# Optimization experiments

Hardware: AMD Instinct MI355X
Metric: run time of the kernel (lower is better)

## Reference

```python
import jax, jax.numpy as jnp
import numpy as np

TEMPERATURES = (0.02, 0.05, 0.2)
NORMALIZE_FEATURES = True
NORMALIZE_DRIFT = True
EPS = 1e-8


def _sqdist(a, b):
    # ||a_i - b_j||^2 via expansion; clamp tiny negatives from fp error
    aa = jnp.sum(a * a, axis=1)[:, None]
    bb = jnp.sum(b * b, axis=1)[None, :]
    return jnp.maximum(aa + bb - 2.0 * (a @ b.T), 0.0)


def compute_drifting_field(x, y_pos, y_neg, temperatures):
    """Multi-scale RBF-kernel drifting field.

    V(x) = mean_tau [ softmax_j(-d(x,y_pos_j)/tau) @ y_pos
                    - softmax_k(-d(x,y_neg_k)/tau) @ y_neg ]
    (the attraction/repulsion (y - x) terms: the -x cancels between pos and neg)
    Returns (V, raw_drift_norm, lambda_V).
    """
    D = x.shape[1]
    if NORMALIZE_FEATURES:
        # scale-invariant distances: global RMS of the reference samples
        ref = jnp.concatenate([y_pos, y_neg], axis=0)
        scale = jnp.sqrt(jnp.mean(ref * ref) + EPS)
    else:
        scale = jnp.asarray(1.0, x.dtype)
    xs, yp, yn = x / scale, y_pos / scale, y_neg / scale

    d_pos = _sqdist(xs, yp)  # [N, N_pos]
    d_neg = _sqdist(xs, yn)  # [N, N_neg]

    V = jnp.zeros_like(xs)
    for tau in temperatures:
        w_pos = jax.nn.softmax(-d_pos / tau, axis=1)
        w_neg = jax.nn.softmax(-d_neg / tau, axis=1)
        V = V + (w_pos @ yp - w_neg @ yn)
    V = (V / len(temperatures)) * scale  # back to original feature scale

    raw_drift_norm = jnp.mean(jnp.sum(V * V, axis=1))  # E[||V_raw||^2]
    lambda_V = jnp.sqrt(raw_drift_norm / D + EPS)
    if NORMALIZE_DRIFT:
        V = V / lambda_V
    return V, raw_drift_norm, lambda_V


def reference(x, y_pos, y_neg):
    V, raw_drift_norm, lambda_V = compute_drifting_field(x, y_pos, y_neg, TEMPERATURES)
    x_target = jax.lax.stop_gradient(x + V)
    loss_per_sample = jnp.mean((x - x_target) ** 2, axis=1)
    loss = jnp.mean(loss_per_sample)  # reduction='mean'
    drift_norm = jnp.mean(jnp.sum(V * V, axis=1))
    # per-temperature logging: original redundantly recomputes the full field
    per_temp = jnp.stack([
        compute_drifting_field(x, y_pos, y_neg, (tau,))[1] for tau in TEMPERATURES
    ])
    return loss, drift_norm, raw_drift_norm, lambda_V, per_temp, jax.lax.stop_gradient(V)


def setup_inputs() -> dict:
    key = jax.random.key(0)
    k1, k2, k3 = jax.random.split(key, 3)
    N, D = 4096, 256
    return {
        "x": jax.random.normal(k1, (N, D), dtype=jnp.float32),
        "y_pos": jax.random.normal(k2, (N, D), dtype=jnp.float32),
        "y_neg": jax.random.normal(k3, (N, D), dtype=jnp.float32),
    }
```

## Files before the change

### kernel.cpp

```cpp
#include <hip/hip_runtime.h>

#define NPTS 4096
#define DIM  256
#define TIL  64
#define WCAND 32

typedef unsigned short u16;
typedef unsigned long long u64;
typedef __attribute__((ext_vector_type(8))) short bf16x8;
typedef __attribute__((ext_vector_type(4))) float f32x4;
typedef __attribute__((ext_vector_type(4))) unsigned short u16x4;

__device__ __forceinline__ float exp2fast(float x) {
  float r;
  asm("v_exp_f32 %0, %1" : "=v"(r) : "v"(x));
  return r;
}

__device__ __forceinline__ void gload_lds16(const void* g, void* l) {
  __builtin_amdgcn_global_load_lds((const __attribute__((address_space(1))) void*)g,
                                   (__attribute__((address_space(3))) void*)l, 16, 0, 0);
}

__device__ __forceinline__ float blk_sum(float v, float* sh) {
  #pragma unroll
  for (int off = 32; off; off >>= 1) v += __shfl_down(v, off);
  int lane = threadIdx.x & 63, w = threadIdx.x >> 6;
  __syncthreads();
  if (lane == 0) sh[w] = v;
  __syncthreads();
  return sh[0] + sh[1] + sh[2] + sh[3];
}

__global__ __launch_bounds__(256) void split3_kernel(
    const float* __restrict__ x, const float* __restrict__ yp, const float* __restrict__ yn,
    u16* __restrict__ xb, u16* __restrict__ ypb, u16* __restrict__ ynb,
    float* __restrict__ bbp, float* __restrict__ bbn)
{
  const float* src; u16* dst; float* bb;
  if      (blockIdx.y == 0) { src = x;  dst = xb;  bb = nullptr; }
  else if (blockIdx.y == 1) { src = yp; dst = ypb; bb = bbp; }
  else                      { src = yn; dst = ynb; bb = bbn; }

  int lane = threadIdx.x & 63;
  int wave = threadIdx.x >> 6;
  int row  = blockIdx.x * 4 + wave;
  const float4 v = *reinterpret_cast<const float4*>(src + (size_t)row * DIM + lane * 4);
  float xs[4] = {v.x, v.y, v.z, v.w};
  u16x4 h;
  float ss = 0.f;
  #pragma unroll
  for (int e = 0; e < 4; ++e) {
    unsigned b = __float_as_uint(xs[e]);
    h[e] = (u16)((b + 0x7fffu + ((b >> 16) & 1u)) >> 16);
    ss += xs[e] * xs[e];
  }
  *reinterpret_cast<u16x4*>(dst + (size_t)row * DIM + lane * 4) = h;
  if (bb) {
    #pragma unroll
    for (int off = 32; off; off >>= 1) ss += __shfl_down(ss, off);
    if (lane == 0) bb[row] = ss;
  }
}

__global__ __launch_bounds__(256) void reduce_ss(
    const float* __restrict__ bbp, const float* __restrict__ bbn, float* __restrict__ accums)
{
  __shared__ float red[4];
  int tid = threadIdx.x;
  float s = 0.f;
  for (int k = tid; k < NPTS; k += 256) s += bbp[k] + bbn[k];
  s = blk_sum(s, red);
  if (tid == 0) accums[0] = s;
}

__global__ __launch_bounds__(256, 4) void gemm_kernel(
    const u16* __restrict__ Xb, const u16* __restrict__ Ypb, const u16* __restrict__ Ynb,
    const float* __restrict__ bbp, const float* __restrict__ bbn,
    const float* __restrict__ accums,
    float* __restrict__ M, u64* __restrict__ Kmask)
{
  __shared__ u16 Ah[2][128 * 32];
  __shared__ u16 Bh[2][128 * 32];

  const int side = blockIdx.z;
  const u16* Yb = side ? Ynb : Ypb;
  const float* bbv = side ? bbn : bbp;

  const int tid  = threadIdx.x;
  const int lane = tid & 63;
  const int wave = tid >> 6;
  const int wm = wave >> 1, wn = wave & 1;
  const int l15 = lane & 15, lhi = lane >> 4;

  const int rf = blockIdx.x * 128;
  const int cf = blockIdx.y * 128;
  const int til = blockIdx.y * 2 + wn;

  const int r0  = tid >> 2;
  const int pc0 = tid & 3;
  const int r1  = (tid + 256) >> 2;
  const int pc1 = tid & 3;

  f32x4 acc[4][4] = {};

  {
    int gc0 = pc0 ^ (r0 & 3), gc1 = pc1 ^ (r1 & 3);
    gload_lds16(Xb + (size_t)(rf + r0) * DIM + gc0 * 8, Ah[0] + r0 * 32 + pc0 * 8);
    gload_lds16(Yb + (size_t)(cf + r0) * DIM + gc0 * 8, Bh[0] + r0 * 32 + pc0 * 8);
    gload_lds16(Xb + (size_t)(rf + r1) * DIM + gc1 * 8, Ah[0] + r1 * 32 + pc1 * 8);
    gload_lds16(Yb + (size_t)(cf + r1) * DIM + gc1 * 8, Bh[0] + r1 * 32 + pc1 * 8);
  }

  #pragma unroll 2
  for (int ks = 0; ks < 8; ++ks) {
    const int cur = ks & 1;
    if (ks < 7) asm volatile("s_waitcnt vmcnt(4)" ::: "memory");
    else        asm volatile("s_waitcnt vmcnt(0)" ::: "memory");
    __builtin_amdgcn_s_barrier();

    if (ks < 7) {
      int ko = (ks + 1) * 32;
      int gc0 = pc0 ^ (r0 & 3), gc1 = pc1 ^ (r1 & 3);
      gload_lds16(Xb + (size_t)(rf + r0) * DIM + ko + gc0 * 8, Ah[cur ^ 1] + r0 * 32 + pc0 * 8);
      gload_lds16(Yb + (size_t)(cf + r0) * DIM + ko + gc0 * 8, Bh[cur ^ 1] + r0 * 32 + pc0 * 8);
      gload_lds16(Xb + (size_t)(rf + r1) * DIM + ko + gc1 * 8, Ah[cur ^ 1] + r1 * 32 + pc1 * 8);
      gload_lds16(Yb + (size_t)(cf + r1) * DIM + ko + gc1 * 8, Bh[cur ^ 1] + r1 * 32 + pc1 * 8);
    }

    bf16x8 a[4], b[4];
    #pragma unroll
    for (int mi = 0; mi < 4; ++mi) {
      int R = wm * 64 + mi * 16 + l15;
      a[mi] = *reinterpret_cast<const bf16x8*>(Ah[cur] + R * 32 + ((lhi ^ (R & 3)) * 8));
    }
    #pragma unroll
    for (int ni = 0; ni < 4; ++ni) {
      int R = wn * 64 + ni * 16 + l15;
      b[ni] = *reinterpret_cast<const bf16x8*>(Bh[cur] + R * 32 + ((lhi ^ (R & 3)) * 8));
    }
    #pragma unroll
    for (int mi = 0; mi < 4; ++mi)
      #pragma unroll
      for (int ni = 0; ni < 4; ++ni)
        acc[mi][ni] = __builtin_amdgcn_mfma_f32_16x16x32_bf16(a[mi], b[ni], acc[mi][ni], 0, 0, 0);
  }

  const float scalesq = accums[0] * (1.0f / (2.0f * NPTS * DIM)) + 1e-8f;
  const float thrP = 30.0f * scalesq * 0.2f + 2.5f * scalesq + 0.5f;

  float bbc[4];
  #pragma unroll
  for (int ni = 0; ni < 4; ++ni) bbc[ni] = bbv[cf + wn * 64 + ni * 16 + l15];

  #pragma unroll
  for (int mi = 0; mi < 4; ++mi)
    #pragma unroll
    for (int r = 0; r < 4; ++r) {
      float uv[4];
      float mx = -3.0e38f;
      #pragma unroll
      for (int ni = 0; ni < 4; ++ni) {
        uv[ni] = 2.0f * acc[mi][ni][r] - bbc[ni];
        mx = fmaxf(mx, uv[ni]);
      }
      #pragma unroll
      for (int off = 1; off < 16; off <<= 1) mx = fmaxf(mx, __shfl_xor(mx, off));
      const float cut = mx - thrP;

      u64 bal[4];
      #pragma unroll
      for (int ni = 0; ni < 4; ++ni) bal[ni] = __ballot(uv[ni] > cut);

      u64 mask = 0;
      #pragma unroll
      for (int ni = 0; ni < 4; ++ni)
        mask |= ((bal[ni] >> (lhi * 16)) & 0xFFFFull) << (ni * 16);

      const int rowG = rf + wm * 64 + mi * 16 + lhi * 4 + r;
      if (l15 == 0) {
        Kmask[((size_t)side * TIL + til) * NPTS + rowG] = mask;
        M[((size_t)side * NPTS + rowG) * TIL + til] = mx;
      }
    }
}

__global__ __launch_bounds__(256) void row_kernel(
    const float* __restrict__ M, const u64* __restrict__ Kmask,
    const float* __restrict__ bbp, const float* __restrict__ bbn,
    const float* __restrict__ x,
    const float* __restrict__ ypos, const float* __restrict__ yneg,
    const float* __restrict__ accums, float* __restrict__ parts,
    float* __restrict__ Vout)
{
  __shared__ unsigned cl[4][WCAND];

  const int tid  = threadIdx.x;
  const int lane = tid & 63;
  const int w    = tid >> 6;
  const int row  = blockIdx.x * 4 + w;

  const float scalesq = accums[0] * (1.0f / (2.0f * NPTS * DIM)) + 1e-8f;
  const float L2E = 1.4426950408889634f;
  const float c0 = L2E / (scalesq * 0.02f);
  const float c1 = L2E / (scalesq * 0.05f);
  const float c2 = L2E / (scalesq * 0.2f);
  const float thrP = 30.0f * scalesq * 0.2f + 2.5f * scalesq + 0.5f;

  const f32x4 xv = *reinterpret_cast<const f32x4*>(x + (size_t)row * DIM + lane * 4);

  f32x4 V0 = {0,0,0,0}, V1 = {0,0,0,0}, V2 = {0,0,0,0};

  for (int side = 0; side < 2; ++side) {
    const float* bb = side ? bbn : bbp;
    const float* y  = side ? yneg : ypos;
    const float sgn = side ? -1.f : 1.f;

    float Mv = M[((size_t)side * NPTS + row) * TIL + lane];
    float g = Mv;
    #pragma unroll
    for (int off = 32; off; off >>= 1) g = fmaxf(g, __shfl_xor(g, off));
    const float cut = g - thrP;

    u64 mm = __ballot(Mv > cut);
    int nc = 0;
    while (mm) {
      int t = __ffsll((long long)mm) - 1;
      mm &= mm - 1;
      u64 mask = Kmask[((size_t)side * TIL + t) * NPTS + row];
      bool keep = (mask >> lane) & 1ull;
      int rank = __popcll(mask & ((1ull << lane) - 1ull));
      if (keep && nc + rank < WCAND) cl[w][nc + rank] = t * 64 + lane;
      nc += __popcll(mask);
    }
    nc = nc < WCAND ? nc : WCAND;

    float me = -3.0e38f, p0 = 0.f, p1 = 0.f, p2 = 0.f;
    f32x4 A0 = {0,0,0,0}, A1 = {0,0,0,0}, A2 = {0,0,0,0};
    for (int bs = 0; bs < nc; bs += 8) {
      const int rem = nc - bs;
      int jq[8];
      f32x4 yv[8];
      float dq[8], uq[8];
      #pragma unroll
      for (int q = 0; q < 8; ++q) {
        int idx = (q < rem) ? bs + q : bs;
        jq[q] = (int)cl[w][idx];
        yv[q] = *reinterpret_cast<const f32x4*>(y + (size_t)jq[q] * DIM + lane * 4);
      }
      #pragma unroll
      for (int q = 0; q < 8; ++q)
        dq[q] = xv[0]*yv[q][0] + xv[1]*yv[q][1] + xv[2]*yv[q][2] + xv[3]*yv[q][3];
      #pragma unroll
      for (int off = 32; off; off >>= 1)
        #pragma unroll
        for (int q = 0; q < 8; ++q) dq[q] += __shfl_xor(dq[q], off);
      #pragma unroll
      for (int q = 0; q < 8; ++q)
        uq[q] = (q < rem) ? 2.0f * dq[q] - bb[jq[q]] : -3.0e38f;

      float cm = uq[0];
      #pragma unroll
      for (int q = 1; q < 8; ++q) cm = fmaxf(cm, uq[q]);
      float nm = fmaxf(me, cm);
      float s0 = exp2fast((me - nm) * c0);
      float s1 = exp2fast((me - nm) * c1);
      float s2 = exp2fast((me - nm) * c2);
      p0 *= s0; p1 *= s1; p2 *= s2;
      A0 *= s0; A1 *= s1; A2 *= s2;
      #pragma unroll
      for (int q = 0; q < 8; ++q) {
        float du = uq[q] - nm;
        float e0 = exp2fast(du * c0);
        float e1 = exp2fast(du * c1);
        float e2 = exp2fast(du * c2);
        p0 += e0; p1 += e1; p2 += e2;
        A0 += e0 * yv[q]; A1 += e1 * yv[q]; A2 += e2 * yv[q];
      }
      me = nm;
    }
    V0 += (sgn / p0) * A0;
    V1 += (sgn / p1) * A1;
    V2 += (sgn / p2) * A2;
  }

  f32x4 vr = (V0 + V1 + V2) * (1.0f / 3.0f);
  *reinterpret_cast<f32x4*>(Vout + (size_t)row * DIM + lane * 4) = vr;

  float s0 = V0[0]*V0[0] + V0[1]*V0[1] + V0[2]*V0[2] + V0[3]*V0[3];
  float s1 = V1[0]*V1[0] + V1[1]*V1[1] + V1[2]*V1[2] + V1[3]*V1[3];
  float s2 = V2[0]*V2[0] + V2[1]*V2[1] + V2[2]*V2[2] + V2[3]*V2[3];
  float sr = vr[0]*vr[0] + vr[1]*vr[1] + vr[2]*vr[2] + vr[3]*vr[3];
  #pragma unroll
  for (int off = 32; off; off >>= 1) {
    s0 += __shfl_xor(s0, off);
    s1 += __shfl_xor(s1, off);
    s2 += __shfl_xor(s2, off);
    sr += __shfl_xor(sr, off);
  }
  if (lane == 0) {
    parts[row]            = sr;
    parts[NPTS + row]     = s0;
    parts[2 * NPTS + row] = s1;
    parts[3 * NPTS + row] = s2;
  }
}

__global__ __launch_bounds__(256) void reduce_parts(
    const float* __restrict__ parts, float* __restrict__ accums)
{
  __shared__ float red[4];
  int tid = threadIdx.x;
  #pragma unroll
  for (int a = 0; a < 4; ++a) {
    float s = 0.f;
    for (int k = tid; k < NPTS; k += 256) s += parts[a * NPTS + k];
    s = blk_sum(s, red);
    if (tid == 0) accums[1 + a] = s;
  }
}

__global__ __launch_bounds__(256) void final_kernel(
    const float* __restrict__ accums, float* __restrict__ out)
{
  float raw  = accums[1] * (1.0f / NPTS);
  float lam2 = raw * (1.0f / DIM) + 1e-8f;
  float lam  = sqrtf(lam2);
  float inv  = 1.0f / lam;
  size_t idx = (size_t)blockIdx.x * 256 + threadIdx.x;
  out[7 + idx] *= inv;
  if (blockIdx.x == 0 && threadIdx.x == 0) {
    float drift = raw / lam2;
    out[0] = drift * (1.0f / DIM);
    out[1] = drift;
    out[2] = raw;
    out[3] = lam;
    out[4] = accums[2] * (1.0f / NPTS);
    out[5] = accums[3] * (1.0f / NPTS);
    out[6] = accums[4] * (1.0f / NPTS);
  }
}

extern "C" void kernel_launch(void* const* d_in, const int* in_sizes, int n_in,
                              void* d_out, int out_size, void* d_ws, size_t ws_size,
                              hipStream_t stream)
{
  (void)in_sizes; (void)n_in; (void)out_size; (void)ws_size;
  const float* x    = (const float*)d_in[0];
  const float* ypos = (const float*)d_in[1];
  const float* yneg = (const float*)d_in[2];
  float* out = (float*)d_out;
  char* ws = (char*)d_ws;

  float* accums = (float*)ws;
  float* bbp    = (float*)(ws + 256);
  float* bbn    = (float*)(ws + 16640);
  float* parts  = (float*)(ws + 33024);
  float* M      = (float*)(ws + 98560);
  u64*   Kmask  = (u64*)(ws + 98560 + 2097152);
  u16* xb  = (u16*)(ws + 98560 + 2097152 + 4194304);
  u16* ypb = xb + (size_t)NPTS * DIM;
  u16* ynb = xb + 2 * (size_t)NPTS * DIM;

  split3_kernel<<<dim3(NPTS / 4, 3), 256, 0, stream>>>(x, ypos, yneg, xb, ypb, ynb, bbp, bbn);
  reduce_ss<<<1, 256, 0, stream>>>(bbp, bbn, accums);
  gemm_kernel<<<dim3(32, 32, 2), 256, 0, stream>>>(xb, ypb, ynb, bbp, bbn, accums, M, Kmask);
  row_kernel<<<NPTS / 4, 256, 0, stream>>>(M, Kmask, bbp, bbn, x, ypos, yneg,
                                           accums, parts, out + 7);
  reduce_parts<<<1, 256, 0, stream>>>(parts, accums);
  final_kernel<<<NPTS, 256, 0, stream>>>(accums, out);
}
```

Before: 86.36 us.

## Fold reduction kernels into consumers, triple-buffer GEMM loads, swizzle block order

Drops the single-block reduce_ss and reduce_parts launches. Each GEMM and row block now redundantly sums the 8192 row norms to get the scale, and final_kernel recomputes the drift-norm reduction in every block. The GEMM moves from double to triple-buffered LDS with a two-stage prefetch, lowers the occupancy hint from 4 to 3, and remaps block IDs for better L2 locality. The aim is fewer serialized tiny launches and better latency hiding, at the cost of redundant reduction work in every block and more LDS per block.

```diff
diff --git a/kernel.cpp b/kernel.cpp
--- a/kernel.cpp
+++ b/kernel.cpp
@@ -30,6 +30,19 @@
   if (lane == 0) sh[w] = v;
   __syncthreads();
   return sh[0] + sh[1] + sh[2] + sh[3];
+}
+
+__device__ __forceinline__ float block_scalesq(
+    const float* __restrict__ bbp, const float* __restrict__ bbn, float* red, int tid) {
+  float s = 0.f;
+  #pragma unroll
+  for (int q = 0; q < 4; ++q) {
+    f32x4 a = *reinterpret_cast<const f32x4*>(bbp + (q * 256 + tid) * 4);
+    f32x4 b = *reinterpret_cast<const f32x4*>(bbn + (q * 256 + tid) * 4);
+    s += a[0] + a[1] + a[2] + a[3] + b[0] + b[1] + b[2] + b[3];
+  }
+  float tot = blk_sum(s, red);
+  return tot * (1.0f / (2.0f * NPTS * DIM)) + 1e-8f;
 }
 
 __global__ __launch_bounds__(256) void split3_kernel(
@@ -63,70 +76,64 @@
   }
 }
 
-__global__ __launch_bounds__(256) void reduce_ss(
-    const float* __restrict__ bbp, const float* __restrict__ bbn, float* __restrict__ accums)
-{
-  __shared__ float red[4];
-  int tid = threadIdx.x;
-  float s = 0.f;
-  for (int k = tid; k < NPTS; k += 256) s += bbp[k] + bbn[k];
-  s = blk_sum(s, red);
-  if (tid == 0) accums[0] = s;
-}
-
-__global__ __launch_bounds__(256, 4) void gemm_kernel(
+__global__ __launch_bounds__(256, 3) void gemm_kernel(
     const u16* __restrict__ Xb, const u16* __restrict__ Ypb, const u16* __restrict__ Ynb,
     const float* __restrict__ bbp, const float* __restrict__ bbn,
-    const float* __restrict__ accums,
     float* __restrict__ M, u64* __restrict__ Kmask)
 {
-  __shared__ u16 Ah[2][128 * 32];
-  __shared__ u16 Bh[2][128 * 32];
-
-  const int side = blockIdx.z;
+  __shared__ u16 Ah[3][128 * 32];
+  __shared__ u16 Bh[3][128 * 32];
+  __shared__ float red[4];
+
+  const int tid  = threadIdx.x;
+
+  const unsigned lid = blockIdx.x + (blockIdx.y << 5) + (blockIdx.z << 10);
+  const unsigned swz = (lid & 7) * 256 + (lid >> 3);
+  const int bx = swz & 31, by = (swz >> 5) & 31, side = (int)(swz >> 10);
+
   const u16* Yb = side ? Ynb : Ypb;
   const float* bbv = side ? bbn : bbp;
 
-  const int tid  = threadIdx.x;
+  const float scalesq = block_scalesq(bbp, bbn, red, tid);
+
   const int lane = tid & 63;
   const int wave = tid >> 6;
   const int wm = wave >> 1, wn = wave & 1;
   const int l15 = lane & 15, lhi = lane >> 4;
 
-  const int rf = blockIdx.x * 128;
-  const int cf = blockIdx.y * 128;
-  const int til = blockIdx.y * 2 + wn;
+  const int rf = bx * 128;
+  const int cf = by * 128;
+  const int til = by * 2 + wn;
 
   const int r0  = tid >> 2;
-  const int pc0 = tid & 3;
   const int r1  = (tid + 256) >> 2;
-  const int pc1 = tid & 3;
+  const int pc  = tid & 3;
+  const int gc0 = pc ^ (r0 & 3);
+  const int gc1 = pc ^ (r1 & 3);
 
   f32x4 acc[4][4] = {};
 
-  {
-    int gc0 = pc0 ^ (r0 & 3), gc1 = pc1 ^ (r1 & 3);
-    gload_lds16(Xb + (size_t)(rf + r0) * DIM + gc0 * 8, Ah[0] + r0 * 32 + pc0 * 8);
-    gload_lds16(Yb + (size_t)(cf + r0) * DIM + gc0 * 8, Bh[0] + r0 * 32 + pc0 * 8);
-    gload_lds16(Xb + (size_t)(rf + r1) * DIM + gc1 * 8, Ah[0] + r1 * 32 + pc1 * 8);
-    gload_lds16(Yb + (size_t)(cf + r1) * DIM + gc1 * 8, Bh[0] + r1 * 32 + pc1 * 8);
-  }
-
-  #pragma unroll 2
+#define STAGE(KS, BUF)                                                                    \
+  do {                                                                                    \
+    int ko_ = (KS) * 32;                                                                  \
+    gload_lds16(Xb + (size_t)(rf + r0) * DIM + ko_ + gc0 * 8, Ah[BUF] + r0 * 32 + pc * 8);\
+    gload_lds16(Yb + (size_t)(cf + r0) * DIM + ko_ + gc0 * 8, Bh[BUF] + r0 * 32 + pc * 8);\
+    gload_lds16(Xb + (size_t)(rf + r1) * DIM + ko_ + gc1 * 8, Ah[BUF] + r1 * 32 + pc * 8);\
+    gload_lds16(Yb + (size_t)(cf + r1) * DIM + ko_ + gc1 * 8, Bh[BUF] + r1 * 32 + pc * 8);\
+  } while (0)
+
+  STAGE(0, 0);
+  STAGE(1, 1);
+
+  #pragma unroll 1
   for (int ks = 0; ks < 8; ++ks) {
-    const int cur = ks & 1;
+    const int cur = ks % 3;
     if (ks < 7) asm volatile("s_waitcnt vmcnt(4)" ::: "memory");
     else        asm volatile("s_waitcnt vmcnt(0)" ::: "memory");
     __builtin_amdgcn_s_barrier();
-
-    if (ks < 7) {
-      int ko = (ks + 1) * 32;
-      int gc0 = pc0 ^ (r0 & 3), gc1 = pc1 ^ (r1 & 3);
-      gload_lds16(Xb + (size_t)(rf + r0) * DIM + ko + gc0 * 8, Ah[cur ^ 1] + r0 * 32 + pc0 * 8);
-      gload_lds16(Yb + (size_t)(cf + r0) * DIM + ko + gc0 * 8, Bh[cur ^ 1] + r0 * 32 + pc0 * 8);
-      gload_lds16(Xb + (size_t)(rf + r1) * DIM + ko + gc1 * 8, Ah[cur ^ 1] + r1 * 32 + pc1 * 8);
-      gload_lds16(Yb + (size_t)(cf + r1) * DIM + ko + gc1 * 8, Bh[cur ^ 1] + r1 * 32 + pc1 * 8);
-    }
+    __builtin_amdgcn_sched_barrier(0);
+
+    if (ks < 6) STAGE(ks + 2, (ks + 2) % 3);
 
     bf16x8 a[4], b[4];
     #pragma unroll
@@ -145,8 +152,8 @@
       for (int ni = 0; ni < 4; ++ni)
         acc[mi][ni] = __builtin_amdgcn_mfma_f32_16x16x32_bf16(a[mi], b[ni], acc[mi][ni], 0, 0, 0);
   }
-
-  const float scalesq = accums[0] * (1.0f / (2.0f * NPTS * DIM)) + 1e-8f;
+#undef STAGE
+
   const float thrP = 30.0f * scalesq * 0.2f + 2.5f * scalesq + 0.5f;
 
   float bbc[4];
@@ -190,17 +197,17 @@
     const float* __restrict__ bbp, const float* __restrict__ bbn,
     const float* __restrict__ x,
     const float* __restrict__ ypos, const float* __restrict__ yneg,
-    const float* __restrict__ accums, float* __restrict__ parts,
-    float* __restrict__ Vout)
+    float* __restrict__ parts, float* __restrict__ Vout)
 {
   __shared__ unsigned cl[4][WCAND];
+  __shared__ float red[4];
 
   const int tid  = threadIdx.x;
   const int lane = tid & 63;
   const int w    = tid >> 6;
   const int row  = blockIdx.x * 4 + w;
 
-  const float scalesq = accums[0] * (1.0f / (2.0f * NPTS * DIM)) + 1e-8f;
+  const float scalesq = block_scalesq(bbp, bbn, red, tid);
   const float L2E = 1.4426950408889634f;
   const float c0 = L2E / (scalesq * 0.02f);
   const float c1 = L2E / (scalesq * 0.05f);
@@ -306,38 +313,37 @@
   }
 }
 
-__global__ __launch_bounds__(256) void reduce_parts(
-    const float* __restrict__ parts, float* __restrict__ accums)
+__global__ __launch_bounds__(256) void final_kernel(
+    const float* __restrict__ parts, float* __restrict__ out)
 {
   __shared__ float red[4];
-  int tid = threadIdx.x;
-  #pragma unroll
-  for (int a = 0; a < 4; ++a) {
-    float s = 0.f;
-    for (int k = tid; k < NPTS; k += 256) s += parts[a * NPTS + k];
-    s = blk_sum(s, red);
-    if (tid == 0) accums[1 + a] = s;
-  }
-}
-
-__global__ __launch_bounds__(256) void final_kernel(
-    const float* __restrict__ accums, float* __restrict__ out)
-{
-  float raw  = accums[1] * (1.0f / NPTS);
+  const int tid = threadIdx.x;
+
+  float s = 0.f;
+  for (int k = tid; k < NPTS; k += 256) s += parts[k];
+  float raw = blk_sum(s, red) * (1.0f / NPTS);
   float lam2 = raw * (1.0f / DIM) + 1e-8f;
   float lam  = sqrtf(lam2);
   float inv  = 1.0f / lam;
-  size_t idx = (size_t)blockIdx.x * 256 + threadIdx.x;
+
+  int idx = blockIdx.x * 256 + tid;
   out[7 + idx] *= inv;
-  if (blockIdx.x == 0 && threadIdx.x == 0) {
-    float drift = raw / lam2;
-    out[0] = drift * (1.0f / DIM);
-    out[1] = drift;
-    out[2] = raw;
-    out[3] = lam;
-    out[4] = accums[2] * (1.0f / NPTS);
-    out[5] = accums[3] * (1.0f / NPTS);
-    out[6] = accums[4] * (1.0f / NPTS);
+
+  if (blockIdx.x == 0) {
+    #pragma unroll
+    for (int a = 1; a <= 3; ++a) {
+      float t = 0.f;
+      for (int k = tid; k < NPTS; k += 256) t += parts[a * NPTS + k];
+      t = blk_sum(t, red);
+      if (tid == 0) out[3 + a] = t * (1.0f / NPTS);
+    }
+    if (tid == 0) {
+      float drift = raw / lam2;
+      out[0] = drift * (1.0f / DIM);
+      out[1] = drift;
+      out[2] = raw;
+      out[3] = lam;
+    }
   }
 }
 
@@ -352,21 +358,18 @@
   float* out = (float*)d_out;
   char* ws = (char*)d_ws;
 
-  float* accums = (float*)ws;
-  float* bbp    = (float*)(ws + 256);
-  float* bbn    = (float*)(ws + 16640);
-  float* parts  = (float*)(ws + 33024);
-  float* M      = (float*)(ws + 98560);
-  u64*   Kmask  = (u64*)(ws + 98560 + 2097152);
-  u16* xb  = (u16*)(ws + 98560 + 2097152 + 4194304);
+  float* bbp   = (float*)ws;
+  float* bbn   = (float*)(ws + 16384);
+  float* parts = (float*)(ws + 32768);
+  float* M     = (float*)(ws + 98304);
+  u64*   Kmask = (u64*)(ws + 98304 + 2097152);
+  u16* xb  = (u16*)(ws + 98304 + 2097152 + 4194304);
   u16* ypb = xb + (size_t)NPTS * DIM;
   u16* ynb = xb + 2 * (size_t)NPTS * DIM;
 
   split3_kernel<<<dim3(NPTS / 4, 3), 256, 0, stream>>>(x, ypos, yneg, xb, ypb, ynb, bbp, bbn);
-  reduce_ss<<<1, 256, 0, stream>>>(bbp, bbn, accums);
-  gemm_kernel<<<dim3(32, 32, 2), 256, 0, stream>>>(xb, ypb, ynb, bbp, bbn, accums, M, Kmask);
+  gemm_kernel<<<dim3(32, 32, 2), 256, 0, stream>>>(xb, ypb, ynb, bbp, bbn, M, Kmask);
   row_kernel<<<NPTS / 4, 256, 0, stream>>>(M, Kmask, bbp, bbn, x, ypos, yneg,
-                                           accums, parts, out + 7);
-  reduce_parts<<<1, 256, 0, stream>>>(parts, accums);
-  final_kernel<<<NPTS, 256, 0, stream>>>(accums, out);
-}
+                                           parts, out + 7);
+  final_kernel<<<NPTS, 256, 0, stream>>>(parts, out);
+}
```

After: 83.35 us. 3.5% less time.
